# Kernel tuning notes

Measured on AMD Instinct MI355X. Metric: run time of the kernel, lower is better.

Reference implementation:

```python
import jax, jax.numpy as jnp
import numpy as np

N_ATOMS = 200_000
N_EDGES = 6_400_000
N_IMAGES = 128


def setup_inputs() -> dict:
    key = jax.random.key(0)
    k1, k2, k3, k4, k5 = jax.random.split(key, 5)
    edge_diff = jax.random.normal(k1, (N_EDGES, 3), dtype=jnp.float32)
    dE_ddiff = jax.random.normal(k2, (N_EDGES, 3), dtype=jnp.float32)
    # cells: perturbed identity cells so volumes are well-conditioned
    cell = jnp.eye(3, dtype=jnp.float32) * 10.0 + 0.1 * jax.random.normal(
        k3, (N_IMAGES, 3, 3), dtype=jnp.float32)
    edge_idx = jax.random.randint(k4, (N_EDGES, 2), 0, N_ATOMS, dtype=jnp.int64)
    image_idx = jnp.sort(jax.random.randint(k5, (N_ATOMS,), 0, N_IMAGES, dtype=jnp.int64))
    return {"edge_diff": edge_diff, "dE_ddiff": dE_ddiff, "cell": cell,
            "edge_idx": edge_idx, "image_idx": image_idx}


def reference(edge_diff, dE_ddiff, cell, edge_idx, image_idx):
    idx_i = edge_idx[:, 0]
    idx_j = edge_idx[:, 1]
    # forces: scatter-add +dE to i atoms and -dE to j atoms
    i_forces = jax.ops.segment_sum(dE_ddiff, idx_i, num_segments=N_ATOMS)
    j_forces = jax.ops.segment_sum(-dE_ddiff, idx_j, num_segments=N_ATOMS)
    forces = i_forces + j_forces  # [N_ATOMS, 3]
    # per-edge virial outer product, scattered to atoms then to images
    edge_virial = edge_diff[:, :, None] * dE_ddiff[:, None, :]  # [E,3,3]
    atomic_virial = jax.ops.segment_sum(edge_virial, idx_i, num_segments=N_ATOMS)
    virial = jax.ops.segment_sum(atomic_virial, image_idx, num_segments=N_IMAGES)  # [B,3,3]
    # cell volumes: a . (b x c)
    volumes = jnp.sum(cell[:, 0] * jnp.cross(cell[:, 1], cell[:, 2]), axis=-1)  # [B]
    stress = -virial / volumes[:, None, None]
    return forces, virial, stress
```

## Files before the change

kernel.cpp:

```cpp
#include <hip/hip_runtime.h>
#include <hip/hip_fp16.h>


typedef unsigned int uint;
typedef unsigned short ushort;

#define SLICES  256
#define BASHIFT 8
#define NBCAP   1024
#define NVMAX   1152
#define CHUNK_E 2048
#define CHUNK_ENT (2*CHUNK_E)

__device__ __forceinline__ uint pack_h2(float a, float b) {
    const __half2 h = __floats2half2_rn(a, b);
    return *(const uint*)&h;
}

__global__ __launch_bounds__(1024) void k_count(
    const int2* __restrict__ edge_idx, uint* __restrict__ counts,
    int n_edges, int es, int nb)
{
    __shared__ uint hist[NBCAP];
    for (int t = threadIdx.x; t < nb; t += blockDim.x) hist[t] = 0;
    __syncthreads();
    const int s  = blockIdx.x;
    const int e0 = s * es;
    const int e1 = min(n_edges, e0 + es);
    for (int e = e0 + threadIdx.x; e < e1; e += blockDim.x) {
        const int2 ij = edge_idx[e];
        atomicAdd(&hist[((uint)ij.x) >> BASHIFT], 1u);
        atomicAdd(&hist[((uint)ij.y) >> BASHIFT], 1u);
    }
    __syncthreads();
    for (int b = threadIdx.x; b < nb; b += blockDim.x)
        counts[(size_t)b * SLICES + s] = hist[b];
}

__global__ __launch_bounds__(SLICES) void k_rowsum(
    const uint* __restrict__ counts, uint* __restrict__ rowsum)
{
    __shared__ uint red[SLICES];
    const int b = blockIdx.x;
    red[threadIdx.x] = counts[(size_t)b * SLICES + threadIdx.x];
    __syncthreads();
    for (int off = SLICES / 2; off > 0; off >>= 1) {
        if (threadIdx.x < off) red[threadIdx.x] += red[threadIdx.x + off];
        __syncthreads();
    }
    if (threadIdx.x == 0) rowsum[b] = red[0];
}

__global__ __launch_bounds__(1024) void k_scan_rows(
    const uint* __restrict__ rowsum, uint* __restrict__ rowoff, int nb)
{
    __shared__ uint psum[1024];
    const int t = threadIdx.x;
    psum[t] = (t < nb) ? rowsum[t] : 0u;
    __syncthreads();
    for (int off = 1; off < 1024; off <<= 1) {
        uint v = (t >= off) ? psum[t - off] : 0u;
        __syncthreads();
        psum[t] += v;
        __syncthreads();
    }
    if (t < nb) rowoff[t] = (t == 0) ? 0u : psum[t - 1];
}

__global__ __launch_bounds__(SLICES) void k_rowscan(
    uint* __restrict__ counts, const uint* __restrict__ rowoff)
{
    __shared__ uint psum[SLICES];
    const int b = blockIdx.x;
    const int t = threadIdx.x;
    const uint c = counts[(size_t)b * SLICES + t];
    psum[t] = c;
    __syncthreads();
    for (int off = 1; off < SLICES; off <<= 1) {
        uint v = (t >= off) ? psum[t - off] : 0u;
        __syncthreads();
        psum[t] += v;
        __syncthreads();
    }
    counts[(size_t)b * SLICES + t] = rowoff[b] + psum[t] - c;
}

__global__ __launch_bounds__(1024) void k_scatter(
    const float* __restrict__ edge_diff, const float* __restrict__ dE_ddiff,
    const int2* __restrict__ edge_idx,
    const uint* __restrict__ offsets, uint4* __restrict__ entries,
    int n_edges, int es, int nb)
{
    __shared__ uint4 s_ent[CHUNK_ENT];
    __shared__ uint  s_dst[CHUNK_ENT];
    __shared__ uint  cnt[NBCAP];
    __shared__ uint  base[NBCAP];
    __shared__ uint  gcur[NBCAP];
    __shared__ uint  wtot[16], wpre[16];

    const int s    = blockIdx.x;
    const int tid  = threadIdx.x;
    const int lane = tid & 63;
    const int wid  = tid >> 6;

    gcur[tid] = (tid < nb) ? offsets[(size_t)tid * SLICES + s] : 0u;
    __syncthreads();

    const int e0 = s * es;
    const int e1 = min(n_edges, e0 + es);

    for (int clo = e0; clo < e1; clo += CHUNK_E) {
        const int chi  = min(e1, clo + CHUNK_E);
        const int nent = 2 * (chi - clo);

        cnt[tid] = 0;
        __syncthreads();

        uint4 ei[2], ej[2];
        uint  bi[2], bj[2], ri[2], rj[2];
        #pragma unroll
        for (int k = 0; k < 2; ++k) {
            const int e = clo + (k << 10) + tid;
            bi[k] = 0xffffffffu;
            if (e < chi) {
                const int2 ij = edge_idx[e];
                const float dx = dE_ddiff[3*e + 0];
                const float dy = dE_ddiff[3*e + 1];
                const float dz = dE_ddiff[3*e + 2];
                const float ex = edge_diff[3*e + 0];
                const float ey = edge_diff[3*e + 1];
                const float ez = edge_diff[3*e + 2];
                const uint ai = (uint)ij.x, aj = (uint)ij.y;
                bi[k] = ai >> BASHIFT;
                bj[k] = aj >> BASHIFT;
                const uint mask = (1u << BASHIFT) - 1u;
                ei[k].x = pack_h2(dx, dy);
                ei[k].y = (uint)__half_as_ushort(__float2half_rn(dz)) | ((ai & mask) << 16);
                ei[k].z = pack_h2(ex, ey);
                ei[k].w = (uint)__half_as_ushort(__float2half_rn(ez));
                ej[k].x = pack_h2(-dx, -dy);
                ej[k].y = (uint)__half_as_ushort(__float2half_rn(-dz)) | ((aj & mask) << 16);
                ej[k].z = 0u;
                ej[k].w = 0u;
                ri[k] = atomicAdd(&cnt[bi[k]], 1u);
                rj[k] = atomicAdd(&cnt[bj[k]], 1u);
            }
        }
        __syncthreads();

        const uint c0 = cnt[tid];
        uint v = c0;
        #pragma unroll
        for (int off = 1; off < 64; off <<= 1) {
            const uint n = __shfl_up(v, off, 64);
            if (lane >= off) v += n;
        }
        if (lane == 63) wtot[wid] = v;
        __syncthreads();
        if (wid == 0) {
            uint t2 = (lane < 16) ? wtot[lane] : 0u;
            #pragma unroll
            for (int off = 1; off < 16; off <<= 1) {
                const uint n = __shfl_up(t2, off, 64);
                if (lane >= off) t2 += n;
            }
            if (lane < 16) wpre[lane] = t2 - wtot[lane];
        }
        __syncthreads();
        base[tid] = v - c0 + wpre[wid];
        __syncthreads();

        #pragma unroll
        for (int k = 0; k < 2; ++k) {
            if (bi[k] != 0xffffffffu) {
                const uint pi = base[bi[k]] + ri[k];
                s_ent[pi] = ei[k];
                s_dst[pi] = gcur[bi[k]] + ri[k];
                const uint pj = base[bj[k]] + rj[k];
                s_ent[pj] = ej[k];
                s_dst[pj] = gcur[bj[k]] + rj[k];
            }
        }
        __syncthreads();

        for (int t = tid; t < nent; t += 1024)
            entries[s_dst[t]] = s_ent[t];

        gcur[tid] += cnt[tid];
        __syncthreads();
    }
}

__global__ __launch_bounds__(256) void k_gather(
    const uint4* __restrict__ entries, const uint* __restrict__ offsets,
    const int* __restrict__ image_idx,
    float* __restrict__ forces, float* __restrict__ virial ,
    int n_atoms, int nb, uint total)
{
    __shared__ float tile[4][3 << BASHIFT];
    __shared__ int   s_img[1 << BASHIFT];
    __shared__ float redA[4][9], redB[4][9];

    const int q    = blockIdx.x;
    const int tid  = threadIdx.x;
    const int wid  = tid >> 6;
    const int lane = tid & 63;
    const int batom = q << BASHIFT;

    {
        const int a = batom + tid;
        s_img[tid] = (a < n_atoms) ? image_idx[a] : -1;
    }
    for (int t = tid; t < 4 * (3 << BASHIFT); t += blockDim.x)
        ((float*)tile)[t] = 0.f;
    __syncthreads();

    const int nvalid = min(n_atoms - batom, 1 << BASHIFT);
    const int imgA = s_img[0];
    const int imgB = s_img[nvalid - 1];
    const bool hasB = (imgB != imgA);

    float accA[9] = {0,0,0,0,0,0,0,0,0};
    float accB[9] = {0,0,0,0,0,0,0,0,0};

    const uint beg = offsets[(size_t)q * SLICES];
    const uint end = (q + 1 < nb) ? offsets[(size_t)(q + 1) * SLICES] : total;
    float* wt = tile[wid];

    for (uint k = beg + tid; k < end; k += blockDim.x) {
        const uint4 ent = entries[k];
        const float2 dxy = __half22float2(*(const __half2*)&ent.x);
        const float  dz  = __half2float(__ushort_as_half((ushort)(ent.y & 0xffffu)));
        const uint local = (ent.y >> 16) & 0xffu;
        atomicAdd(&wt[local*3 + 0], dxy.x);
        atomicAdd(&wt[local*3 + 1], dxy.y);
        atomicAdd(&wt[local*3 + 2], dz);

        const float2 exy = __half22float2(*(const __half2*)&ent.z);
        const float  ez  = __half2float(__ushort_as_half((ushort)(ent.w & 0xffffu)));
        const int m = s_img[local];
        float p[9];
        p[0] = exy.x*dxy.x; p[1] = exy.x*dxy.y; p[2] = exy.x*dz;
        p[3] = exy.y*dxy.x; p[4] = exy.y*dxy.y; p[5] = exy.y*dz;
        p[6] = ez   *dxy.x; p[7] = ez   *dxy.y; p[8] = ez   *dz;
        const float wA = (m == imgA) ? 1.f : 0.f;
        const float wB = (hasB && m == imgB) ? 1.f : 0.f;
        #pragma unroll
        for (int c = 0; c < 9; ++c) { accA[c] += wA * p[c]; accB[c] += wB * p[c]; }
        if (m != imgA && m != imgB && m >= 0) {
            #pragma unroll
            for (int c = 0; c < 9; ++c) unsafeAtomicAdd(&virial[m*9 + c], p[c]);
        }
    }

    #pragma unroll
    for (int c = 0; c < 9; ++c) {
        float a = accA[c], b = accB[c];
        #pragma unroll
        for (int off = 32; off > 0; off >>= 1) {
            a += __shfl_down(a, off, 64);
            b += __shfl_down(b, off, 64);
        }
        if (lane == 0) { redA[wid][c] = a; redB[wid][c] = b; }
    }
    __syncthreads();
    if (tid < 9) {
        const float sA = redA[0][tid] + redA[1][tid] + redA[2][tid] + redA[3][tid];
        unsafeAtomicAdd(&virial[imgA*9 + tid], sA);
        if (hasB) {
            const float sB = redB[0][tid] + redB[1][tid] + redB[2][tid] + redB[3][tid];
            unsafeAtomicAdd(&virial[imgB*9 + tid], sB);
        }
    }

    const int lim3 = nvalid * 3;
    for (int t = tid; t < lim3; t += blockDim.x)
        forces[(size_t)batom * 3 + t] = tile[0][t] + tile[1][t] + tile[2][t] + tile[3][t];
}

__global__ void k_stress(const float* __restrict__ cell,
                         const float* __restrict__ virial,
                         float* __restrict__ stress, int n_images)
{
    const int t = blockIdx.x * blockDim.x + threadIdx.x;
    if (t >= n_images * 9) return;
    const float* c = &cell[(t / 9) * 9];
    const float crx = c[4]*c[8] - c[5]*c[7];
    const float cry = c[5]*c[6] - c[3]*c[8];
    const float crz = c[3]*c[7] - c[4]*c[6];
    const float vol = c[0]*crx + c[1]*cry + c[2]*crz;
    stress[t] = virial[t] * (-1.0f / vol);
}

__global__ __launch_bounds__(256) void edge_kernel_fb(
    const float* __restrict__ edge_diff, const float* __restrict__ dE_ddiff,
    const int2* __restrict__ edge_idx, const int* __restrict__ image_idx,
    float* __restrict__ forces, float* __restrict__ virial,
    int n_edges, int n_images)
{
    extern __shared__ float lds_v[];
    const int nv = n_images * 9;
    for (int t = threadIdx.x; t < nv; t += blockDim.x) lds_v[t] = 0.f;
    __syncthreads();
    const int stride = gridDim.x * blockDim.x;
    for (int e = blockIdx.x * blockDim.x + threadIdx.x; e < n_edges; e += stride) {
        const int2 ij = edge_idx[e];
        const int i = ij.x, j = ij.y;
        const float dx = dE_ddiff[3*e+0], dy = dE_ddiff[3*e+1], dz = dE_ddiff[3*e+2];
        unsafeAtomicAdd(&forces[3*i+0],  dx);
        unsafeAtomicAdd(&forces[3*i+1],  dy);
        unsafeAtomicAdd(&forces[3*i+2],  dz);
        unsafeAtomicAdd(&forces[3*j+0], -dx);
        unsafeAtomicAdd(&forces[3*j+1], -dy);
        unsafeAtomicAdd(&forces[3*j+2], -dz);
        const float ex = edge_diff[3*e+0], ey = edge_diff[3*e+1], ez = edge_diff[3*e+2];
        float* v = &lds_v[image_idx[i] * 9];
        atomicAdd(&v[0], ex*dx); atomicAdd(&v[1], ex*dy); atomicAdd(&v[2], ex*dz);
        atomicAdd(&v[3], ey*dx); atomicAdd(&v[4], ey*dy); atomicAdd(&v[5], ey*dz);
        atomicAdd(&v[6], ez*dx); atomicAdd(&v[7], ez*dy); atomicAdd(&v[8], ez*dz);
    }
    __syncthreads();
    for (int t = threadIdx.x; t < nv; t += blockDim.x) {
        const float val = lds_v[t];
        if (val != 0.f) unsafeAtomicAdd(&virial[t], val);
    }
}

extern "C" void kernel_launch(void* const* d_in, const int* in_sizes, int n_in,
                              void* d_out, int out_size, void* d_ws, size_t ws_size,
                              hipStream_t stream)
{
    const float* edge_diff = (const float*)d_in[0];
    const float* dE_ddiff  = (const float*)d_in[1];
    const float* cell      = (const float*)d_in[2];
    const int2*  edge_idx  = (const int2*)d_in[3];
    const int*   image_idx = (const int*)d_in[4];

    const int n_edges  = in_sizes[0] / 3;
    const int n_images = in_sizes[2] / 9;
    const int n_atoms  = in_sizes[4];
    const int nv       = n_images * 9;

    float* out    = (float*)d_out;
    float* forces = out;
    float* virial = out + (size_t)n_atoms * 3;
    float* stress = virial + nv;

    const int nb = (n_atoms + (1 << BASHIFT) - 1) >> BASHIFT;
    const int es = (n_edges + SLICES - 1) / SLICES;
    const uint total = (uint)(2 * (size_t)n_edges);

    const size_t entries_bytes = (size_t)total * sizeof(uint4);
    const size_t counts_bytes  = (size_t)nb * SLICES * sizeof(uint);
    const size_t aux_bytes     = 2 * (size_t)NBCAP * sizeof(uint);
    const size_t need = entries_bytes + counts_bytes + aux_bytes;

    if (ws_size >= need && nb <= NBCAP && nv <= NVMAX) {
        uint4* entries = (uint4*)d_ws;
        uint*  offsets = (uint*)((char*)d_ws + entries_bytes);
        uint*  rowsum  = offsets + (size_t)nb * SLICES;
        uint*  rowoff  = rowsum + NBCAP;

        hipMemsetAsync(virial, 0, nv * sizeof(float), stream);

        k_count<<<SLICES, 1024, 0, stream>>>(edge_idx, offsets, n_edges, es, nb);
        k_rowsum<<<nb, SLICES, 0, stream>>>(offsets, rowsum);
        k_scan_rows<<<1, 1024, 0, stream>>>(rowsum, rowoff, nb);
        k_rowscan<<<nb, SLICES, 0, stream>>>(offsets, rowoff);
        k_scatter<<<SLICES, 1024, 0, stream>>>(edge_diff, dE_ddiff, edge_idx,
                                               offsets, entries, n_edges, es, nb);
        k_gather<<<nb, 256, 0, stream>>>(entries, offsets, image_idx,
                                         forces, virial, n_atoms, nb, total);
        k_stress<<<(nv + 255) / 256, 256, 0, stream>>>(cell, virial, stress, n_images);
    } else {
        hipMemsetAsync(out, 0, ((size_t)n_atoms * 3 + nv) * sizeof(float), stream);
        edge_kernel_fb<<<2048, 256, nv * sizeof(float), stream>>>(
            edge_diff, dE_ddiff, edge_idx, image_idx, forces, virial, n_edges, n_images);
        k_stress<<<(nv + 255) / 256, 256, 0, stream>>>(cell, virial, stress, n_images);
    }
}
```

Before: 588.7 us.

## Compute virial in scatter pass via LDS atomics and shrink entries to 8 bytes

Moves the per-edge virial outer product out of the gather kernel and into the scatter kernel, where it is accumulated per image in shared memory with a random image_idx lookup per edge and flushed once per block. The bucketed entries drop from 16 to 8 bytes each, since they no longer carry edge_diff, which halves scatter write and gather read traffic. Slice count doubles to 512, and the gather kernel uses 512 threads with 4-way unrolled loads. The cost is nine LDS float atomics per edge in scatter, possibly contended on a few image slots, plus an extra gather on image_idx.

```diff
diff --git a/kernel.cpp b/kernel.cpp
--- a/kernel.cpp
+++ b/kernel.cpp
@@ -5,12 +5,14 @@
 typedef unsigned int uint;
 typedef unsigned short ushort;
 
-#define SLICES  256
+#define SLICES  512
 #define BASHIFT 8
 #define NBCAP   1024
 #define NVMAX   1152
 #define CHUNK_E 2048
 #define CHUNK_ENT (2*CHUNK_E)
+#define GT      512
+#define GW      (GT/64)
 
 __device__ __forceinline__ uint pack_h2(float a, float b) {
     const __half2 h = __floats2half2_rn(a, b);
@@ -87,15 +89,17 @@
 
 __global__ __launch_bounds__(1024) void k_scatter(
     const float* __restrict__ edge_diff, const float* __restrict__ dE_ddiff,
-    const int2* __restrict__ edge_idx,
-    const uint* __restrict__ offsets, uint4* __restrict__ entries,
-    int n_edges, int es, int nb)
-{
-    __shared__ uint4 s_ent[CHUNK_ENT];
+    const int2* __restrict__ edge_idx, const int* __restrict__ image_idx,
+    const uint* __restrict__ offsets, uint2* __restrict__ entries,
+    float* __restrict__ virial ,
+    int n_edges, int es, int nb, int nv)
+{
+    __shared__ uint2 s_ent[CHUNK_ENT];
     __shared__ uint  s_dst[CHUNK_ENT];
     __shared__ uint  cnt[NBCAP];
     __shared__ uint  base[NBCAP];
     __shared__ uint  gcur[NBCAP];
+    __shared__ float v_lds[NVMAX];
     __shared__ uint  wtot[16], wpre[16];
 
     const int s    = blockIdx.x;
@@ -104,6 +108,7 @@
     const int wid  = tid >> 6;
 
     gcur[tid] = (tid < nb) ? offsets[(size_t)tid * SLICES + s] : 0u;
+    for (int t = tid; t < nv; t += 1024) v_lds[t] = 0.f;
     __syncthreads();
 
     const int e0 = s * es;
@@ -116,7 +121,7 @@
         cnt[tid] = 0;
         __syncthreads();
 
-        uint4 ei[2], ej[2];
+        uint2 ei[2], ej[2];
         uint  bi[2], bj[2], ri[2], rj[2];
         #pragma unroll
         for (int k = 0; k < 2; ++k) {
@@ -127,21 +132,25 @@
                 const float dx = dE_ddiff[3*e + 0];
                 const float dy = dE_ddiff[3*e + 1];
                 const float dz = dE_ddiff[3*e + 2];
-                const float ex = edge_diff[3*e + 0];
-                const float ey = edge_diff[3*e + 1];
-                const float ez = edge_diff[3*e + 2];
                 const uint ai = (uint)ij.x, aj = (uint)ij.y;
                 bi[k] = ai >> BASHIFT;
                 bj[k] = aj >> BASHIFT;
                 const uint mask = (1u << BASHIFT) - 1u;
+                const uint dzh = (uint)__half_as_ushort(__float2half_rn(dz));
                 ei[k].x = pack_h2(dx, dy);
-                ei[k].y = (uint)__half_as_ushort(__float2half_rn(dz)) | ((ai & mask) << 16);
-                ei[k].z = pack_h2(ex, ey);
-                ei[k].w = (uint)__half_as_ushort(__float2half_rn(ez));
-                ej[k].x = pack_h2(-dx, -dy);
-                ej[k].y = (uint)__half_as_ushort(__float2half_rn(-dz)) | ((aj & mask) << 16);
-                ej[k].z = 0u;
-                ej[k].w = 0u;
+                ei[k].y = dzh | ((ai & mask) << 16);
+                ej[k].x = ei[k].x ^ 0x80008000u;
+                ej[k].y = (dzh ^ 0x8000u) | ((aj & mask) << 16);
+
+                const float ex = edge_diff[3*e + 0];
+                const float ey = edge_diff[3*e + 1];
+                const float ez = edge_diff[3*e + 2];
+                const int img = image_idx[ij.x];
+                float* v = &v_lds[img * 9];
+                atomicAdd(&v[0], ex*dx); atomicAdd(&v[1], ex*dy); atomicAdd(&v[2], ex*dz);
+                atomicAdd(&v[3], ey*dx); atomicAdd(&v[4], ey*dy); atomicAdd(&v[5], ey*dz);
+                atomicAdd(&v[6], ez*dx); atomicAdd(&v[7], ez*dy); atomicAdd(&v[8], ez*dz);
+
                 ri[k] = atomicAdd(&cnt[bi[k]], 1u);
                 rj[k] = atomicAdd(&cnt[bj[k]], 1u);
             }
@@ -189,93 +198,66 @@
         gcur[tid] += cnt[tid];
         __syncthreads();
     }
-}
-
-__global__ __launch_bounds__(256) void k_gather(
-    const uint4* __restrict__ entries, const uint* __restrict__ offsets,
-    const int* __restrict__ image_idx,
-    float* __restrict__ forces, float* __restrict__ virial ,
+
+    for (int t = tid; t < nv; t += 1024)
+        unsafeAtomicAdd(&virial[t], v_lds[t]);
+}
+
+__device__ __forceinline__ void proc_entry(uint2 e, float* wt) {
+    const float2 dxy = __half22float2(*(const __half2*)&e.x);
+    const float  dz  = __half2float(__ushort_as_half((ushort)(e.y & 0xffffu)));
+    const uint local = (e.y >> 16) & 0xffu;
+    atomicAdd(&wt[local*3 + 0], dxy.x);
+    atomicAdd(&wt[local*3 + 1], dxy.y);
+    atomicAdd(&wt[local*3 + 2], dz);
+}
+
+__global__ __launch_bounds__(GT) void k_gather(
+    const uint2* __restrict__ entries, const uint* __restrict__ offsets,
+    float* __restrict__ forces,
     int n_atoms, int nb, uint total)
 {
-    __shared__ float tile[4][3 << BASHIFT];
-    __shared__ int   s_img[1 << BASHIFT];
-    __shared__ float redA[4][9], redB[4][9];
+    __shared__ float tile[GW][3 << BASHIFT];
 
     const int q    = blockIdx.x;
     const int tid  = threadIdx.x;
     const int wid  = tid >> 6;
-    const int lane = tid & 63;
     const int batom = q << BASHIFT;
 
-    {
-        const int a = batom + tid;
-        s_img[tid] = (a < n_atoms) ? image_idx[a] : -1;
-    }
-    for (int t = tid; t < 4 * (3 << BASHIFT); t += blockDim.x)
+    for (int t = tid; t < GW * (3 << BASHIFT); t += GT)
         ((float*)tile)[t] = 0.f;
     __syncthreads();
-
-    const int nvalid = min(n_atoms - batom, 1 << BASHIFT);
-    const int imgA = s_img[0];
-    const int imgB = s_img[nvalid - 1];
-    const bool hasB = (imgB != imgA);
-
-    float accA[9] = {0,0,0,0,0,0,0,0,0};
-    float accB[9] = {0,0,0,0,0,0,0,0,0};
 
     const uint beg = offsets[(size_t)q * SLICES];
     const uint end = (q + 1 < nb) ? offsets[(size_t)(q + 1) * SLICES] : total;
     float* wt = tile[wid];
 
-    for (uint k = beg + tid; k < end; k += blockDim.x) {
-        const uint4 ent = entries[k];
-        const float2 dxy = __half22float2(*(const __half2*)&ent.x);
-        const float  dz  = __half2float(__ushort_as_half((ushort)(ent.y & 0xffffu)));
-        const uint local = (ent.y >> 16) & 0xffu;
-        atomicAdd(&wt[local*3 + 0], dxy.x);
-        atomicAdd(&wt[local*3 + 1], dxy.y);
-        atomicAdd(&wt[local*3 + 2], dz);
-
-        const float2 exy = __half22float2(*(const __half2*)&ent.z);
-        const float  ez  = __half2float(__ushort_as_half((ushort)(ent.w & 0xffffu)));
-        const int m = s_img[local];
-        float p[9];
-        p[0] = exy.x*dxy.x; p[1] = exy.x*dxy.y; p[2] = exy.x*dz;
-        p[3] = exy.y*dxy.x; p[4] = exy.y*dxy.y; p[5] = exy.y*dz;
-        p[6] = ez   *dxy.x; p[7] = ez   *dxy.y; p[8] = ez   *dz;
-        const float wA = (m == imgA) ? 1.f : 0.f;
-        const float wB = (hasB && m == imgB) ? 1.f : 0.f;
+    const uint step = GT;
+    uint k = beg + tid;
+    while (k + 3u * step < end) {
+        const uint2 e0 = entries[k];
+        const uint2 e1 = entries[k +      step];
+        const uint2 e2 = entries[k + 2u * step];
+        const uint2 e3 = entries[k + 3u * step];
+        proc_entry(e0, wt);
+        proc_entry(e1, wt);
+        proc_entry(e2, wt);
+        proc_entry(e3, wt);
+        k += 4u * step;
+    }
+    for (; k < end; k += step)
+        proc_entry(entries[k], wt);
+
+    __syncthreads();
+
+    const int nvalid = min(n_atoms - batom, 1 << BASHIFT);
+    const int lim3 = nvalid * 3;
+    for (int t = tid; t < lim3; t += GT) {
+        float ssum = 0.f;
         #pragma unroll
-        for (int c = 0; c < 9; ++c) { accA[c] += wA * p[c]; accB[c] += wB * p[c]; }
-        if (m != imgA && m != imgB && m >= 0) {
-            #pragma unroll
-            for (int c = 0; c < 9; ++c) unsafeAtomicAdd(&virial[m*9 + c], p[c]);
-        }
-    }
-
-    #pragma unroll
-    for (int c = 0; c < 9; ++c) {
-        float a = accA[c], b = accB[c];
-        #pragma unroll
-        for (int off = 32; off > 0; off >>= 1) {
-            a += __shfl_down(a, off, 64);
-            b += __shfl_down(b, off, 64);
-        }
-        if (lane == 0) { redA[wid][c] = a; redB[wid][c] = b; }
-    }
-    __syncthreads();
-    if (tid < 9) {
-        const float sA = redA[0][tid] + redA[1][tid] + redA[2][tid] + redA[3][tid];
-        unsafeAtomicAdd(&virial[imgA*9 + tid], sA);
-        if (hasB) {
-            const float sB = redB[0][tid] + redB[1][tid] + redB[2][tid] + redB[3][tid];
-            unsafeAtomicAdd(&virial[imgB*9 + tid], sB);
-        }
-    }
-
-    const int lim3 = nvalid * 3;
-    for (int t = tid; t < lim3; t += blockDim.x)
-        forces[(size_t)batom * 3 + t] = tile[0][t] + tile[1][t] + tile[2][t] + tile[3][t];
+        for (int w = 0; w < GW; ++w) ssum += tile[w][t];
+        forces[(size_t)batom * 3 + t] = ssum;
+    }
 }
 
 __global__ void k_stress(const float* __restrict__ cell,
@@ -350,13 +332,13 @@
     const int es = (n_edges + SLICES - 1) / SLICES;
     const uint total = (uint)(2 * (size_t)n_edges);
 
-    const size_t entries_bytes = (size_t)total * sizeof(uint4);
+    const size_t entries_bytes = (size_t)total * sizeof(uint2);
     const size_t counts_bytes  = (size_t)nb * SLICES * sizeof(uint);
     const size_t aux_bytes     = 2 * (size_t)NBCAP * sizeof(uint);
     const size_t need = entries_bytes + counts_bytes + aux_bytes;
 
     if (ws_size >= need && nb <= NBCAP && nv <= NVMAX) {
-        uint4* entries = (uint4*)d_ws;
+        uint2* entries = (uint2*)d_ws;
         uint*  offsets = (uint*)((char*)d_ws + entries_bytes);
         uint*  rowsum  = offsets + (size_t)nb * SLICES;
         uint*  rowoff  = rowsum + NBCAP;
@@ -367,10 +349,10 @@
         k_rowsum<<<nb, SLICES, 0, stream>>>(offsets, rowsum);
         k_scan_rows<<<1, 1024, 0, stream>>>(rowsum, rowoff, nb);
         k_rowscan<<<nb, SLICES, 0, stream>>>(offsets, rowoff);
-        k_scatter<<<SLICES, 1024, 0, stream>>>(edge_diff, dE_ddiff, edge_idx,
-                                               offsets, entries, n_edges, es, nb);
-        k_gather<<<nb, 256, 0, stream>>>(entries, offsets, image_idx,
-                                         forces, virial, n_atoms, nb, total);
+        k_scatter<<<SLICES, 1024, 0, stream>>>(edge_diff, dE_ddiff, edge_idx, image_idx,
+                                               offsets, entries, virial,
+                                               n_edges, es, nb, nv);
+        k_gather<<<nb, GT, 0, stream>>>(entries, offsets, forces, n_atoms, nb, total);
         k_stress<<<(nv + 255) / 256, 256, 0, stream>>>(cell, virial, stress, n_images);
     } else {
         hipMemsetAsync(out, 0, ((size_t)n_atoms * 3 + nv) * sizeof(float), stream);
```

Result: slower. 770.2 us (+30.8%).
